# Performance work log

Measured on AMD Instinct MI355X. Metric: run time of the kernel, lower is better.

Reference implementation:

```python
import jax, jax.numpy as jnp
import numpy as np

N_NODES = 16384
N_FEAT = 16384
EMBED = 64
BATCH = 4096
N_EDGES = 524288


def setup_inputs() -> dict:
    key = jax.random.key(0)
    k1, k2, k3, k4, k5 = jax.random.split(key, 5)
    x = jax.random.randint(k1, (BATCH, 2), 0, N_NODES, dtype=jnp.int64)
    X = jax.random.normal(k2, (N_NODES, N_FEAT), dtype=jnp.float32) * 0.05
    edge_index = jax.random.randint(k3, (2, N_EDGES), 0, N_NODES, dtype=jnp.int64)
    W_gcn = jax.random.normal(k4, (N_FEAT, EMBED), dtype=jnp.float32) * (1.0 / np.sqrt(N_FEAT))
    b_gcn = jnp.zeros((EMBED,), dtype=jnp.float32)
    w_lin = jax.random.normal(k5, (N_NODES, 1), dtype=jnp.float32) * 0.01
    b_lin = jnp.zeros((1,), dtype=jnp.float32)
    return {"x": x, "X": X, "edge_index": edge_index, "W_gcn": W_gcn,
            "b_gcn": b_gcn, "w_lin": w_lin, "b_lin": b_lin}


def _gcn_conv(X, edge_index, W, b):
    """PyG GCNConv: symmetric-normalized aggregation with self-loops."""
    n = X.shape[0]
    xw = X @ W  # [N, D] -- dominant GEMM
    loop = jnp.arange(n)
    src = jnp.concatenate([edge_index[0], loop])
    dst = jnp.concatenate([edge_index[1], loop])
    deg = jax.ops.segment_sum(jnp.ones_like(dst, dtype=xw.dtype), dst, num_segments=n)
    dinv = jnp.where(deg > 0, jax.lax.rsqrt(deg), 0.0)
    norm = dinv[src] * dinv[dst]  # [E+N]
    out = jax.ops.segment_sum(xw[src] * norm[:, None], dst, num_segments=n)
    return out + b


def reference(x, X, edge_index, W_gcn, b_gcn, w_lin, b_lin):
    emb_all = _gcn_conv(X, edge_index, W_gcn, b_gcn)  # [N, D]
    emb = emb_all[x]  # [B, 2, D]
    # FM pairwise interaction: 0.5 * sum((sum_i v)^2 - sum_i v^2)
    sq_of_sum = jnp.sum(emb, axis=1) ** 2       # [B, D]
    sum_of_sq = jnp.sum(emb ** 2, axis=1)       # [B, D]
    fm = 0.5 * jnp.sum(sq_of_sum - sum_of_sq, axis=1, keepdims=True)  # [B, 1]
    lin = jnp.sum(w_lin[x], axis=1) + b_lin      # [B, 1]
    return (lin + fm).squeeze(1)                 # [B]
```

## Files before the change

kernel.cpp:

```cpp
#include <hip/hip_runtime.h>
#include <cstddef>

#define N_NODES 16384
#define N_FEAT  16384
#define EMBED   64
#define BATCH   4096
#define N_EDGES 524288

typedef __attribute__((ext_vector_type(8))) short bf16x8;
typedef __attribute__((ext_vector_type(4))) float f32x4;

__device__ __forceinline__ ushort f32_to_bf16(float f) {
    unsigned u = __float_as_uint(f);
    return (ushort)((u + 0x7FFFu + ((u >> 16) & 1u)) >> 16);
}
__device__ __forceinline__ float bf16_to_f32(ushort h) {
    return __uint_as_float((unsigned)h << 16);
}

__device__ __forceinline__ void split8(float4 a, float4 b, bf16x8& h, bf16x8& l) {
    float f[8] = {a.x, a.y, a.z, a.w, b.x, b.y, b.z, b.w};
    #pragma unroll
    for (int j = 0; j < 8; ++j) {
        ushort hh = f32_to_bf16(f[j]);
        h[j] = (short)hh;
        l[j] = (short)f32_to_bf16(f[j] - bf16_to_f32(hh));
    }
}

__global__ void k_deg_init(float* __restrict__ deg) {
    int n = blockIdx.x * blockDim.x + threadIdx.x;
    if (n < N_NODES) deg[n] = 1.0f;
}
__global__ void k_deg_acc(const int* __restrict__ ei, float* __restrict__ deg) {
    int e = blockIdx.x * blockDim.x + threadIdx.x;
    if (e < N_EDGES) atomicAdd(&deg[ei[N_EDGES + e]], 1.0f);
}
__global__ void k_dinv(float* __restrict__ deg) {
    int n = blockIdx.x * blockDim.x + threadIdx.x;
    if (n < N_NODES) deg[n] = rsqrtf(deg[n]);
}

__global__ __launch_bounds__(1024) void k_scan(const float* __restrict__ deg,
                                               int* __restrict__ off,
                                               int* __restrict__ cur) {
    __shared__ int part[1024];
    const int t = threadIdx.x;
    int c[16];
    int s = 0;
    #pragma unroll
    for (int i = 0; i < 16; ++i) {
        c[i] = (int)deg[t * 16 + i] - 1;
        s += c[i];
    }
    part[t] = s;
    __syncthreads();
    for (int d = 1; d < 1024; d <<= 1) {
        int v = (t >= d) ? part[t - d] : 0;
        __syncthreads();
        part[t] += v;
        __syncthreads();
    }
    int run = (t == 0) ? 0 : part[t - 1];
    #pragma unroll
    for (int i = 0; i < 16; ++i) {
        off[t * 16 + i] = run;
        cur[t * 16 + i] = run;
        run += c[i];
    }
    if (t == 1023) off[N_NODES] = run;
}

__global__ void k_scatter(const int* __restrict__ ei, int* __restrict__ cur,
                          int* __restrict__ srcs) {
    int e = blockIdx.x * blockDim.x + threadIdx.x;
    if (e < N_EDGES) {
        int s = ei[e];
        int d = ei[N_EDGES + e];
        srcs[atomicAdd(&cur[d], 1)] = s;
    }
}

__global__ void k_wpack(const float* __restrict__ W, short* __restrict__ Wpk) {
    int tid = blockIdx.x * blockDim.x + threadIdx.x;
    int lane = tid & 63;
    int f = tid >> 6;
    int ct = f & 3;
    int ks = (f >> 2) & 511;
    int sp = f >> 11;
    int n = ct * 16 + (lane & 15);
    int kbase = ks * 32 + (lane >> 4) * 8;
    bf16x8 r;
    #pragma unroll
    for (int j = 0; j < 8; ++j) {
        float w = W[(size_t)(kbase + j) * EMBED + n];
        ushort h = f32_to_bf16(w);
        r[j] = (sp == 0) ? (short)h : (short)f32_to_bf16(w - bf16_to_f32(h));
    }
    *(bf16x8*)(Wpk + (size_t)f * 512 + lane * 8) = r;
}

#define GBM 128
#define KSPLIT 8
#define KCHUNK (N_FEAT / KSPLIT)
#define NSTEP (KCHUNK / 32)

__global__ __launch_bounds__(256, 4) void k_gemm(const float* __restrict__ X,
                                                 const short* __restrict__ Wpk,
                                                 float* __restrict__ xw_part) {
    __shared__ float Xs[2][GBM][32];

    const int t = threadIdx.x;
    const int kpl = blockIdx.x & 7;
    const int rb = blockIdx.x >> 3;
    const int block_row = rb * GBM;
    const int w = t >> 6;
    const int lane = t & 63;
    const int g = lane >> 4;
    const int lr = lane & 15;
    const int swz = lr & 7;

    const int rsub = lane >> 3;
    const int qsrc = (lane & 7) ^ rsub;
    const float* gl = X + (size_t)(block_row + w * 32 + rsub) * N_FEAT
                        + (size_t)kpl * KCHUNK + qsrc * 4;

    f32x4 acc[2][4] = {};
    int cur = 0;

#define STAGE(buf, kt)                                                          \
    {                                                                           \
        _Pragma("unroll")                                                       \
        for (int i = 0; i < 4; ++i)                                             \
            __builtin_amdgcn_global_load_lds(                                   \
                (const __attribute__((address_space(1))) void*)                 \
                    (gl + (size_t)i * 8 * N_FEAT + (kt) * 32),                  \
                (__attribute__((address_space(3))) void*)&Xs[buf][w * 32 + i * 8][0], \
                16, 0, 0);                                                      \
    }

    STAGE(0, 0);
    __syncthreads();

    for (int kt = 0; kt < NSTEP; ++kt) {
        if (kt + 1 < NSTEP) STAGE(cur ^ 1, kt + 1);

        const int kstep = kpl * NSTEP + kt;
        const short* bp = Wpk + (size_t)(kstep * 4) * 512 + lane * 8;
        bf16x8 bh[4], bl[4];
        #pragma unroll
        for (int ct = 0; ct < 4; ++ct) {
            bh[ct] = *(const bf16x8*)(bp + ct * 512);
            bl[ct] = *(const bf16x8*)(bp + ct * 512 + 1048576);
        }

        const int q0 = ((2 * g) ^ swz) * 4;
        const int q1 = ((2 * g + 1) ^ swz) * 4;
        const int r0 = w * 32 + lr;
        float4 x0 = *(const float4*)&Xs[cur][r0][q0];
        float4 x1 = *(const float4*)&Xs[cur][r0][q1];
        float4 x2 = *(const float4*)&Xs[cur][r0 + 16][q0];
        float4 x3 = *(const float4*)&Xs[cur][r0 + 16][q1];
        bf16x8 ah[2], al[2];
        split8(x0, x1, ah[0], al[0]);
        split8(x2, x3, ah[1], al[1]);

        #pragma unroll
        for (int rt = 0; rt < 2; ++rt) {
            #pragma unroll
            for (int ct = 0; ct < 4; ++ct) {
                acc[rt][ct] = __builtin_amdgcn_mfma_f32_16x16x32_bf16(ah[rt], bh[ct], acc[rt][ct], 0, 0, 0);
                acc[rt][ct] = __builtin_amdgcn_mfma_f32_16x16x32_bf16(ah[rt], bl[ct], acc[rt][ct], 0, 0, 0);
                acc[rt][ct] = __builtin_amdgcn_mfma_f32_16x16x32_bf16(al[rt], bh[ct], acc[rt][ct], 0, 0, 0);
            }
        }
        __syncthreads();
        cur ^= 1;
    }
#undef STAGE

    float* part = xw_part + (size_t)kpl * (N_NODES * EMBED);
    #pragma unroll
    for (int rt = 0; rt < 2; ++rt)
        #pragma unroll
        for (int ct = 0; ct < 4; ++ct)
            #pragma unroll
            for (int r = 0; r < 4; ++r) {
                int row = block_row + w * 32 + rt * 16 + g * 4 + r;
                part[(size_t)row * EMBED + ct * 16 + lr] = acc[rt][ct][r];
            }
}

__global__ void k_reduce(const float4* __restrict__ part, float4* __restrict__ xw) {
    int i = blockIdx.x * blockDim.x + threadIdx.x;
    float4 s = part[i];
    #pragma unroll
    for (int p = 1; p < KSPLIT; ++p) {
        float4 v = part[(size_t)p * (N_NODES * EMBED / 4) + i];
        s.x += v.x; s.y += v.y; s.z += v.z; s.w += v.w;
    }
    xw[i] = s;
}

__global__ void k_gather(const int* __restrict__ off, const int* __restrict__ srcs,
                         const float* __restrict__ xw, const float* __restrict__ dinv,
                         float* __restrict__ agg) {
    int n = blockIdx.x * 4 + (threadIdx.x >> 6);
    int lane = threadIdx.x & 63;
    float dn = dinv[n];
    float acc = xw[(size_t)n * EMBED + lane] * dn;
    int i = off[n], i1 = off[n + 1];
    for (; i + 1 < i1; i += 2) {
        int s0 = srcs[i], s1 = srcs[i + 1];
        float a0 = xw[(size_t)s0 * EMBED + lane] * dinv[s0];
        float a1 = xw[(size_t)s1 * EMBED + lane] * dinv[s1];
        acc += a0 + a1;
    }
    if (i < i1) {
        int s = srcs[i];
        acc += xw[(size_t)s * EMBED + lane] * dinv[s];
    }
    agg[(size_t)n * EMBED + lane] = acc * dn;
}

__global__ void k_final(const int* __restrict__ x, const float* __restrict__ agg,
                        const float* __restrict__ b_gcn, const float* __restrict__ w_lin,
                        const float* __restrict__ b_lin, float* __restrict__ out) {
    int b = blockIdx.x * (blockDim.x >> 6) + (threadIdx.x >> 6);
    int lane = threadIdx.x & 63;
    if (b >= BATCH) return;
    int i0 = x[2 * b + 0];
    int i1 = x[2 * b + 1];
    float bg = b_gcn[lane];
    float e0 = agg[(size_t)i0 * EMBED + lane] + bg;
    float e1 = agg[(size_t)i1 * EMBED + lane] + bg;
    float p = e0 * e1;
    #pragma unroll
    for (int off = 32; off > 0; off >>= 1) p += __shfl_down(p, off, 64);
    if (lane == 0) out[b] = p + w_lin[i0] + w_lin[i1] + b_lin[0];
}

extern "C" void kernel_launch(void* const* d_in, const int* in_sizes, int n_in,
                              void* d_out, int out_size, void* d_ws, size_t ws_size,
                              hipStream_t stream) {
    (void)in_sizes; (void)n_in; (void)out_size; (void)ws_size;

    const int*   x   = (const int*)d_in[0];
    const float* X   = (const float*)d_in[1];
    const int*   ei  = (const int*)d_in[2];
    const float* W   = (const float*)d_in[3];
    const float* bg  = (const float*)d_in[4];
    const float* wl  = (const float*)d_in[5];
    const float* bl  = (const float*)d_in[6];
    float* out = (float*)d_out;

    char* ws = (char*)d_ws;
    float* xw      = (float*)(ws);
    short* Wpk     = (short*)(ws + (size_t)(4 << 20));
    float* agg     = (float*)(ws + (size_t)(4 << 20));
    float* dinv    = (float*)(ws + (size_t)(8 << 20));
    int*   off     = (int*)  (ws + (size_t)(8 << 20) + (1 << 17));
    int*   cur     = (int*)  (ws + (size_t)(8 << 20) + (1 << 18));
    int*   srcs    = (int*)  (ws + (size_t)(8 << 20) + (1 << 19));
    float* xw_part = (float*)(ws + (size_t)(16 << 20));

    k_deg_init<<<N_NODES / 256, 256, 0, stream>>>(dinv);
    k_deg_acc<<<N_EDGES / 256, 256, 0, stream>>>(ei, dinv);
    k_scan<<<1, 1024, 0, stream>>>(dinv, off, cur);
    k_dinv<<<N_NODES / 256, 256, 0, stream>>>(dinv);
    k_scatter<<<N_EDGES / 256, 256, 0, stream>>>(ei, cur, srcs);

    k_wpack<<<1024, 256, 0, stream>>>(W, Wpk);
    k_gemm<<<(N_NODES / GBM) * KSPLIT, 256, 0, stream>>>(X, Wpk, xw_part);
    k_reduce<<<(N_NODES * EMBED / 4) / 256, 256, 0, stream>>>((const float4*)xw_part, (float4*)xw);

    k_gather<<<N_NODES / 4, 256, 0, stream>>>(off, srcs, xw, dinv, agg);
    k_final<<<BATCH / 4, 256, 0, stream>>>(x, agg, bg, wl, bl, out);
}
```

Before: 1.501 ms.

## Load GEMM X tiles directly into registers instead of staging through LDS

The GEMM kernel stops staging X through double-buffered shared memory with global_load_lds and barriers. Each thread now reads its A fragment straight from global memory into registers, with a two-step register prefetch. The block row tile shrinks from 128 to 64 rows, so the grid doubles and each wave handles one 16-row tile instead of two. This removes LDS traffic and __syncthreads, but each thread's global reads are now 32-byte segments strided by a full row, and every B fragment is reused over half as many rows.

```diff
diff --git a/kernel.cpp b/kernel.cpp
--- a/kernel.cpp
+++ b/kernel.cpp
@@ -100,7 +100,6 @@
     *(bf16x8*)(Wpk + (size_t)f * 512 + lane * 8) = r;
 }
 
-#define GBM 128
 #define KSPLIT 8
 #define KCHUNK (N_FEAT / KSPLIT)
 #define NSTEP (KCHUNK / 32)
@@ -108,87 +107,78 @@
 __global__ __launch_bounds__(256, 4) void k_gemm(const float* __restrict__ X,
                                                  const short* __restrict__ Wpk,
                                                  float* __restrict__ xw_part) {
-    __shared__ float Xs[2][GBM][32];
-
     const int t = threadIdx.x;
     const int kpl = blockIdx.x & 7;
-    const int rb = blockIdx.x >> 3;
-    const int block_row = rb * GBM;
+    const int rb  = blockIdx.x >> 3;
     const int w = t >> 6;
     const int lane = t & 63;
     const int g = lane >> 4;
     const int lr = lane & 15;
-    const int swz = lr & 7;
-
-    const int rsub = lane >> 3;
-    const int qsrc = (lane & 7) ^ rsub;
-    const float* gl = X + (size_t)(block_row + w * 32 + rsub) * N_FEAT
-                        + (size_t)kpl * KCHUNK + qsrc * 4;
-
-    f32x4 acc[2][4] = {};
-    int cur = 0;
-
-#define STAGE(buf, kt)                                                          \
-    {                                                                           \
-        _Pragma("unroll")                                                       \
-        for (int i = 0; i < 4; ++i)                                             \
-            __builtin_amdgcn_global_load_lds(                                   \
-                (const __attribute__((address_space(1))) void*)                 \
-                    (gl + (size_t)i * 8 * N_FEAT + (kt) * 32),                  \
-                (__attribute__((address_space(3))) void*)&Xs[buf][w * 32 + i * 8][0], \
-                16, 0, 0);                                                      \
-    }
-
-    STAGE(0, 0);
-    __syncthreads();
-
-    for (int kt = 0; kt < NSTEP; ++kt) {
-        if (kt + 1 < NSTEP) STAGE(cur ^ 1, kt + 1);
-
-        const int kstep = kpl * NSTEP + kt;
-        const short* bp = Wpk + (size_t)(kstep * 4) * 512 + lane * 8;
-        bf16x8 bh[4], bl[4];
+
+    const float* ap = X + (size_t)(rb * 64 + w * 16 + lr) * N_FEAT
+                        + (size_t)kpl * KCHUNK + g * 8;
+    const short* bp0 = Wpk + (size_t)(kpl * NSTEP * 4) * 512 + lane * 8;
+
+    f32x4 acc[4] = {};
+
+    float4 a0_0 = *(const float4*)(ap);
+    float4 a0_1 = *(const float4*)(ap + 4);
+    float4 a1_0 = *(const float4*)(ap + 32);
+    float4 a1_1 = *(const float4*)(ap + 36);
+
+    for (int kt = 0; kt < NSTEP; kt += 2) {
+        {
+            const short* bp = bp0 + (size_t)kt * 2048;
+            bf16x8 bh[4], bl[4];
+            #pragma unroll
+            for (int ct = 0; ct < 4; ++ct) {
+                bh[ct] = *(const bf16x8*)(bp + ct * 512);
+                bl[ct] = *(const bf16x8*)(bp + ct * 512 + 1048576);
+            }
+            bf16x8 ah, al;
+            split8(a0_0, a0_1, ah, al);
+            if (kt + 2 < NSTEP) {
+                a0_0 = *(const float4*)(ap + (size_t)(kt + 2) * 32);
+                a0_1 = *(const float4*)(ap + (size_t)(kt + 2) * 32 + 4);
+            }
+            #pragma unroll
+            for (int ct = 0; ct < 4; ++ct) {
+                acc[ct] = __builtin_amdgcn_mfma_f32_16x16x32_bf16(ah, bh[ct], acc[ct], 0, 0, 0);
+                acc[ct] = __builtin_amdgcn_mfma_f32_16x16x32_bf16(ah, bl[ct], acc[ct], 0, 0, 0);
+                acc[ct] = __builtin_amdgcn_mfma_f32_16x16x32_bf16(al, bh[ct], acc[ct], 0, 0, 0);
+            }
+        }
+        {
+            const short* bp = bp0 + (size_t)(kt + 1) * 2048;
+            bf16x8 bh[4], bl[4];
+            #pragma unroll
+            for (int ct = 0; ct < 4; ++ct) {
+                bh[ct] = *(const bf16x8*)(bp + ct * 512);
+                bl[ct] = *(const bf16x8*)(bp + ct * 512 + 1048576);
+            }
+            bf16x8 ah, al;
+            split8(a1_0, a1_1, ah, al);
+            if (kt + 3 < NSTEP) {
+                a1_0 = *(const float4*)(ap + (size_t)(kt + 3) * 32);
+                a1_1 = *(const float4*)(ap + (size_t)(kt + 3) * 32 + 4);
+            }
+            #pragma unroll
+            for (int ct = 0; ct < 4; ++ct) {
+                acc[ct] = __builtin_amdgcn_mfma_f32_16x16x32_bf16(ah, bh[ct], acc[ct], 0, 0, 0);
+                acc[ct] = __builtin_amdgcn_mfma_f32_16x16x32_bf16(ah, bl[ct], acc[ct], 0, 0, 0);
+                acc[ct] = __builtin_amdgcn_mfma_f32_16x16x32_bf16(al, bh[ct], acc[ct], 0, 0, 0);
+            }
+        }
+    }
+
+    float* part = xw_part + (size_t)kpl * (N_NODES * EMBED);
+    #pragma unroll
+    for (int ct = 0; ct < 4; ++ct)
         #pragma unroll
-        for (int ct = 0; ct < 4; ++ct) {
-            bh[ct] = *(const bf16x8*)(bp + ct * 512);
-            bl[ct] = *(const bf16x8*)(bp + ct * 512 + 1048576);
+        for (int r = 0; r < 4; ++r) {
+            int row = rb * 64 + w * 16 + g * 4 + r;
+            part[(size_t)row * EMBED + ct * 16 + lr] = acc[ct][r];
         }
-
-        const int q0 = ((2 * g) ^ swz) * 4;
-        const int q1 = ((2 * g + 1) ^ swz) * 4;
-        const int r0 = w * 32 + lr;
-        float4 x0 = *(const float4*)&Xs[cur][r0][q0];
-        float4 x1 = *(const float4*)&Xs[cur][r0][q1];
-        float4 x2 = *(const float4*)&Xs[cur][r0 + 16][q0];
-        float4 x3 = *(const float4*)&Xs[cur][r0 + 16][q1];
-        bf16x8 ah[2], al[2];
-        split8(x0, x1, ah[0], al[0]);
-        split8(x2, x3, ah[1], al[1]);
-
-        #pragma unroll
-        for (int rt = 0; rt < 2; ++rt) {
-            #pragma unroll
-            for (int ct = 0; ct < 4; ++ct) {
-                acc[rt][ct] = __builtin_amdgcn_mfma_f32_16x16x32_bf16(ah[rt], bh[ct], acc[rt][ct], 0, 0, 0);
-                acc[rt][ct] = __builtin_amdgcn_mfma_f32_16x16x32_bf16(ah[rt], bl[ct], acc[rt][ct], 0, 0, 0);
-                acc[rt][ct] = __builtin_amdgcn_mfma_f32_16x16x32_bf16(al[rt], bh[ct], acc[rt][ct], 0, 0, 0);
-            }
-        }
-        __syncthreads();
-        cur ^= 1;
-    }
-#undef STAGE
-
-    float* part = xw_part + (size_t)kpl * (N_NODES * EMBED);
-    #pragma unroll
-    for (int rt = 0; rt < 2; ++rt)
-        #pragma unroll
-        for (int ct = 0; ct < 4; ++ct)
-            #pragma unroll
-            for (int r = 0; r < 4; ++r) {
-                int row = block_row + w * 32 + rt * 16 + g * 4 + r;
-                part[(size_t)row * EMBED + ct * 16 + lr] = acc[rt][ct][r];
-            }
 }
 
 __global__ void k_reduce(const float4* __restrict__ part, float4* __restrict__ xw) {
@@ -271,7 +261,7 @@
     k_scatter<<<N_EDGES / 256, 256, 0, stream>>>(ei, cur, srcs);
 
     k_wpack<<<1024, 256, 0, stream>>>(W, Wpk);
-    k_gemm<<<(N_NODES / GBM) * KSPLIT, 256, 0, stream>>>(X, Wpk, xw_part);
+    k_gemm<<<(N_NODES / 64) * KSPLIT, 256, 0, stream>>>(X, Wpk, xw_part);
     k_reduce<<<(N_NODES * EMBED / 4) / 256, 256, 0, stream>>>((const float4*)xw_part, (float4*)xw);
 
     k_gather<<<N_NODES / 4, 256, 0, stream>>>(off, srcs, xw, dinv, agg);
```

After: 1.592 ms. 1.06x slower.
